# Optimization experiments

Measured on AMD Instinct MI355X. Metric: run time of the kernel, lower is better.

The kernel has to match this reference:

```python
import jax, jax.numpy as jnp
import numpy as np

H = 1024        # hidden_size
NH = 16         # num_heads
HD = H // NH    # head_dim
NS = 3          # num_strata


def setup_inputs() -> dict:
    key = jax.random.key(0)
    ks = jax.random.split(key, 12)
    s = 1.0 / np.sqrt(H)
    inp = {
        "hidden_states": jax.random.normal(ks[0], (2, 2048, H), dtype=jnp.float32),
        "Wq": jax.random.uniform(ks[1], (H, H), minval=-s, maxval=s, dtype=jnp.float32),
        "bq": jax.random.uniform(ks[2], (H,), minval=-s, maxval=s, dtype=jnp.float32),
        "Wk": jax.random.uniform(ks[3], (H, H), minval=-s, maxval=s, dtype=jnp.float32),
        "bk": jax.random.uniform(ks[4], (H,), minval=-s, maxval=s, dtype=jnp.float32),
        "Wv": jax.random.uniform(ks[5], (H, H), minval=-s, maxval=s, dtype=jnp.float32),
        "bv": jax.random.uniform(ks[6], (H,), minval=-s, maxval=s, dtype=jnp.float32),
        "Ws": jax.random.uniform(ks[7], (NS, H, H), minval=-s, maxval=s, dtype=jnp.float32),
        "bs": jax.random.uniform(ks[8], (NS, H), minval=-s, maxval=s, dtype=jnp.float32),
        "Wo": jax.random.uniform(ks[9], (H, H), minval=-s, maxval=s, dtype=jnp.float32),
        "bo": jax.random.uniform(ks[10], (H,), minval=-s, maxval=s, dtype=jnp.float32),
    }
    return inp


def reference(hidden_states, Wq, bq, Wk, bk, Wv, bv, Ws, bs, Wo, bo):
    B, S, _ = hidden_states.shape
    # torch nn.Linear: y = x @ W.T + b
    q = hidden_states @ Wq.T + bq
    k = hidden_states @ Wk.T + bk
    v = hidden_states @ Wv.T + bv
    # [B, NH, S, HD]
    q = q.reshape(B, S, NH, HD).transpose(0, 2, 1, 3)
    k = k.reshape(B, S, NH, HD).transpose(0, 2, 1, 3)
    v = v.reshape(B, S, NH, HD).transpose(0, 2, 1, 3)
    scores = jnp.einsum('bhqd,bhkd->bhqk', q, k) / jnp.sqrt(jnp.float32(HD))
    attn = jax.nn.softmax(scores, axis=-1)
    out = jnp.einsum('bhqk,bhkd->bhqd', attn, v)
    attn_output = out.transpose(0, 2, 1, 3).reshape(B, S, H)
    # stratum projections, averaged: [NS, B, S, H] -> mean over strata
    strata = jnp.einsum('bsh,ngh->nbsg', attn_output, Ws) + bs[:, None, None, :]
    enhanced = strata.mean(axis=0)
    output = enhanced @ Wo.T + bo
    return output
```

## Files before the change

kernel.cpp:

```cpp
#include <hip/hip_runtime.h>
#include <stdint.h>

typedef __attribute__((ext_vector_type(8))) short short8;
typedef __attribute__((ext_vector_type(4))) short short4v;
typedef __attribute__((ext_vector_type(4))) float f32x4;
typedef __attribute__((ext_vector_type(16))) float f32x16;
typedef __attribute__((ext_vector_type(2))) unsigned int u32x2;
typedef __attribute__((ext_vector_type(4))) unsigned int u32x4;
typedef unsigned int u32;
typedef const __attribute__((address_space(1))) u32* gas_ptr;
typedef __attribute__((address_space(3))) u32* las_ptr;

#define QSCALE 0.18033688011112042f

__device__ inline short f2bf(float x) {
    u32 u = __float_as_uint(x);
    u = u + 0x7FFFu + ((u >> 16) & 1u);
    return (short)(u >> 16);
}
__device__ inline void gload16(const void* g, const void* l) {
    __builtin_amdgcn_global_load_lds((gas_ptr)g, (las_ptr)l, 16, 0, 0);
}

__global__ __launch_bounds__(256) void prep(const float* __restrict__ X,
                                            const float* __restrict__ Wq,
                                            const float* __restrict__ Wk,
                                            const float* __restrict__ Wv,
                                            const float* __restrict__ Wo,
                                            const float* __restrict__ Ws,
                                            const float* __restrict__ bs,
                                            const float* __restrict__ bo,
                                            short* __restrict__ Xb,
                                            short* __restrict__ Wcat,
                                            short* __restrict__ Wob,
                                            short* __restrict__ WmT,
                                            float* __restrict__ bc) {
    __shared__ short T[64][65];
    const int tid = threadIdx.x;
    const int bid = blockIdx.x;
    if (bid < 2048) {
#pragma unroll
        for (int c = 0; c < 4; c++) {
            const int chunk = bid * 4 + c;
            const float* src;
            short* dst;
            int rel;
            if (chunk < 4096)      { src = X;  dst = Xb;                rel = chunk; }
            else if (chunk < 5120) { src = Wq; dst = Wcat;              rel = chunk - 4096; }
            else if (chunk < 6144) { src = Wk; dst = Wcat + (1 << 20);  rel = chunk - 5120; }
            else if (chunk < 7168) { src = Wv; dst = Wcat + (2 << 20);  rel = chunk - 6144; }
            else                   { src = Wo; dst = Wob;               rel = chunk - 7168; }
            int i = (rel * 256 + tid) * 4;
            float4 v = *(const float4*)&src[i];
            short4v o;
            o[0] = f2bf(v.x); o[1] = f2bf(v.y); o[2] = f2bf(v.z); o[3] = f2bf(v.w);
            *(short4v*)&dst[i] = o;
        }
    } else if (bid < 2304) {
        const int id = bid - 2048;
        const int gx = (id & 15) * 64, jy = (id >> 4) * 64;
        const int HH = 1 << 20;
        for (int e = tid; e < 4096; e += 256) {
            int j = e >> 6, g = e & 63;
            int idx = (jy + j) * 1024 + gx + g;
            float v = (Ws[idx] + Ws[idx + HH] + Ws[idx + 2 * HH]) * (1.0f / 3.0f);
            T[g][j] = f2bf(v);
        }
        __syncthreads();
        for (int e = tid; e < 4096; e += 256) {
            int g = e >> 6, j = e & 63;
            WmT[(long)(gx + g) * 1024 + jy + j] = T[g][j];
        }
    } else {
        const int lane = tid & 63;
        const int n = (bid - 2304) * 4 + (tid >> 6);
        float acc = 0.0f;
        for (int j0 = 0; j0 < 1024; j0 += 64) {
            int j = j0 + lane;
            float bm = (bs[j] + bs[j + 1024] + bs[j + 2048]) * (1.0f / 3.0f);
            acc += Wo[(long)n * 1024 + j] * bm;
        }
#pragma unroll
        for (int off = 1; off < 64; off <<= 1) acc += __shfl_xor(acc, off, 64);
        if (lane == 0) bc[n] = acc + bo[n];
    }
}

__global__ __launch_bounds__(256) void gemm_qkvwc(const short* __restrict__ Xb,
                                                  const short* __restrict__ Wcat,
                                                  const short* __restrict__ Wob,
                                                  const short* __restrict__ WmT,
                                                  const float* __restrict__ bq,
                                                  const float* __restrict__ bk,
                                                  const float* __restrict__ bv,
                                                  short* __restrict__ Qb,
                                                  short* __restrict__ Kb,
                                                  short* __restrict__ Vt,
                                                  short* __restrict__ Wc) {
    __shared__ short As[64 * 64];
    __shared__ short Bs[128 * 64];
    const int K = 1024;
    const int tid  = threadIdx.x;
    const int lane = tid & 63;
    const int wave = tid >> 6;
    const int quad = lane >> 4;
    const int l16  = lane & 15;
    const int bid = (blockIdx.x & 7) * 208 + (blockIdx.x >> 3);
    const short *A, *W;
    int m0, n0, sel;
    if (bid < 1536) {
        sel = bid >> 9;
        int r = bid & 511;
        m0 = (r >> 3) * 64;
        n0 = (r & 7) * 128;
        A = Xb;
        W = Wcat + (long)sel * (1 << 20);
    } else {
        int w = bid - 1536;
        sel = 3;
        m0 = (w >> 3) * 64;
        n0 = (w & 7) * 128;
        A = Wob;
        W = WmT;
    }
    const int wm = (wave >> 1) * 32;
    const int wn = (wave & 1) * 64;

    f32x4 acc[2][4] = {};
    const int sr = tid >> 3;
    const int scol = (((tid & 7) ^ (sr & 7)) << 3);
    const int fo_a = ((quad ^ (l16 & 7)) << 3);
    const int fo_b = (((4 + quad) ^ (l16 & 7)) << 3);

    for (int k0 = 0; k0 < K; k0 += 64) {
#pragma unroll
        for (int i = 0; i < 2; i++) {
            int r = i * 32 + sr;
            gload16(&A[(long)(m0 + r) * K + k0 + scol], &As[i * 2048 + wave * 512]);
        }
#pragma unroll
        for (int i = 0; i < 4; i++) {
            int r = i * 32 + sr;
            gload16(&W[(long)(n0 + r) * K + k0 + scol], &Bs[i * 2048 + wave * 512]);
        }
        __syncthreads();
        short8 bfr[4][2];
#pragma unroll
        for (int ni = 0; ni < 4; ni++) {
            const int row = wn + ni * 16 + l16;
            bfr[ni][0] = *(short8*)&Bs[row * 64 + fo_a];
            bfr[ni][1] = *(short8*)&Bs[row * 64 + fo_b];
        }
#pragma unroll
        for (int mi = 0; mi < 2; mi++) {
            const int row = wm + mi * 16 + l16;
            short8 af0 = *(short8*)&As[row * 64 + fo_a];
            short8 af1 = *(short8*)&As[row * 64 + fo_b];
#pragma unroll
            for (int ni = 0; ni < 4; ni++) {
                acc[mi][ni] = __builtin_amdgcn_mfma_f32_16x16x32_bf16(af0, bfr[ni][0],
                                                                      acc[mi][ni], 0, 0, 0);
                acc[mi][ni] = __builtin_amdgcn_mfma_f32_16x16x32_bf16(af1, bfr[ni][1],
                                                                      acc[mi][ni], 0, 0, 0);
            }
        }
        __syncthreads();
    }

#pragma unroll
    for (int mi = 0; mi < 2; mi++) {
#pragma unroll
        for (int ni = 0; ni < 4; ni++) {
            const int n = n0 + wn + ni * 16 + l16;
            const int mbase = m0 + wm + mi * 16 + quad * 4;
            float bv2 = 0.0f;
            if (sel == 0) bv2 = bq[n];
            else if (sel == 1) bv2 = bk[n];
            else if (sel == 2) bv2 = bv[n];
            if (sel == 2) {
                short4v pk;
#pragma unroll
                for (int r = 0; r < 4; r++) pk[r] = f2bf(acc[mi][ni][r] + bv2);
                long addr = ((long)(mbase >> 11) << 21) + (long)n * 2048 + (mbase & 2047);
                *(short4v*)&Vt[addr] = pk;
            } else if (sel == 0) {
#pragma unroll
                for (int r = 0; r < 4; r++)
                    Qb[(long)(mbase + r) * 1024 + n] = f2bf((acc[mi][ni][r] + bv2) * QSCALE);
            } else {
                short* C = (sel == 1) ? Kb : Wc;
#pragma unroll
                for (int r = 0; r < 4; r++)
                    C[(long)(mbase + r) * 1024 + n] = f2bf(acc[mi][ni][r] + bv2);
            }
        }
    }
}

__global__ __launch_bounds__(512, 4) void attn_kernel(const short* __restrict__ Q,
                                                      const short* __restrict__ Kb,
                                                      const short* __restrict__ Vt,
                                                      short* __restrict__ O) {
    __shared__ short Ks[2][2][64 * 64];
    __shared__ short Vs[2][64 * 64];
    const int tid   = threadIdx.x;
    const int lane  = tid & 63;
    const int wave  = tid >> 6;
    const int group = wave >> 2;
    const int wv    = wave & 3;
    const int gtid  = tid & 255;
    const int l32   = lane & 31;
    const int hi    = lane >> 5;
    const int sw    = l32 & 7;
    const int q0 = blockIdx.x * 128;
    const int h  = blockIdx.y;
    const int b  = blockIdx.z;

    short8 qB[4];
    {
        const long qbase = (long)(b * 2048 + q0 + wv * 32 + l32) * 1024 + h * 64 + hi * 8;
#pragma unroll
        for (int t = 0; t < 4; t++) qB[t] = *(const short8*)&Q[qbase + t * 16];
    }

    const int sr = gtid >> 3;
    const int scol = (((gtid & 7) ^ (sr & 7)) << 3);
    const short* Kp = Kb + (long)(b * 2048 + group * 1024) * 1024 + h * 64;
    const short* Vp = Vt + ((long)b << 21) + (long)h * 64 * 2048 + group * 1024;

    f32x16 o[2] = {};
    float lsum = 0.0f;

#pragma unroll
    for (int i = 0; i < 2; i++) {
        int r = i * 32 + sr;
        gload16(&Kp[(long)r * 1024 + scol], &Ks[group][0][i * 2048 + wv * 512]);
    }
    __syncthreads();

    for (int kt = 0; kt < 16; kt++) {
        const int cur = kt & 1;
        const int kb = kt * 64;

#pragma unroll
        for (int i = 0; i < 2; i++) {
            int r = i * 32 + sr;
            gload16(&Vp[(long)r * 2048 + kb + scol], &Vs[group][i * 2048 + wv * 512]);
        }

        u32 c0[8], c1[8];
#pragma unroll
        for (int kvt = 0; kvt < 2; kvt++) {
            const int row = kvt * 32 + l32;
            f32x16 st = {};
            __builtin_amdgcn_s_setprio(1);
#pragma unroll
            for (int step = 0; step < 4; step++) {
                short8 ak = *(short8*)&Ks[group][cur][row * 64 + (((step * 2 + hi) ^ sw) << 3)];
                st = __builtin_amdgcn_mfma_f32_32x32x16_bf16(ak, qB[step], st, 0, 0, 0);
            }
            __builtin_amdgcn_s_setprio(0);
#pragma unroll
            for (int g = 0; g < 4; g++) {
                float p0 = __builtin_amdgcn_exp2f(st[g * 4 + 0]);
                float p1 = __builtin_amdgcn_exp2f(st[g * 4 + 1]);
                float p2 = __builtin_amdgcn_exp2f(st[g * 4 + 2]);
                float p3 = __builtin_amdgcn_exp2f(st[g * 4 + 3]);
                lsum += (p0 + p1) + (p2 + p3);
                u32 w0, w1;
                asm("v_cvt_pk_bf16_f32 %0, %1, %2" : "=v"(w0) : "v"(p0), "v"(p1));
                asm("v_cvt_pk_bf16_f32 %0, %1, %2" : "=v"(w1) : "v"(p2), "v"(p3));
                c0[kvt * 4 + g] = w0;
                c1[kvt * 4 + g] = w1;
            }
        }

        __syncthreads();

        if (kt < 15) {
            const int kbn = kb + 64;
#pragma unroll
            for (int i = 0; i < 2; i++) {
                int r = i * 32 + sr;
                gload16(&Kp[(long)(kbn + r) * 1024 + scol],
                        &Ks[group][cur ^ 1][i * 2048 + wv * 512]);
            }
        }

        short8 pB[4];
#pragma unroll
        for (int s = 0; s < 4; s++) {
            u32x2 r0 = __builtin_amdgcn_permlane32_swap(c0[2 * s], c0[2 * s + 1], false, false);
            u32x2 r1 = __builtin_amdgcn_permlane32_swap(c1[2 * s], c1[2 * s + 1], false, false);
            u32x4 bw;
            bw[0] = r0[0]; bw[1] = r1[0]; bw[2] = r0[1]; bw[3] = r1[1];
            pB[s] = __builtin_bit_cast(short8, bw);
        }

        __builtin_amdgcn_s_setprio(1);
#pragma unroll
        for (int dt = 0; dt < 2; dt++) {
            const int row = dt * 32 + l32;
#pragma unroll
            for (int s = 0; s < 4; s++) {
                short8 av = *(short8*)&Vs[group][row * 64 + (((s * 2 + hi) ^ sw) << 3)];
                o[dt] = __builtin_amdgcn_mfma_f32_32x32x16_bf16(av, pB[s], o[dt], 0, 0, 0);
            }
        }
        __builtin_amdgcn_s_setprio(0);

        __syncthreads();
    }

    lsum += __shfl_xor(lsum, 32, 64);
    float* cb = (float*)&Ks[0][0][0];
    float* lb = (float*)&Vs[0][0];
    const int ql = wv * 32 + l32;
    if (group == 1) {
#pragma unroll
        for (int dt = 0; dt < 2; dt++) {
#pragma unroll
            for (int g = 0; g < 4; g++) {
                f32x4 v4;
#pragma unroll
                for (int i = 0; i < 4; i++) v4[i] = o[dt][g * 4 + i];
                *(f32x4*)&cb[ql * 64 + dt * 32 + g * 8 + hi * 4] = v4;
            }
        }
        if (hi == 0) lb[ql] = lsum;
    }
    __syncthreads();
    if (group == 0) {
        const float inv = 1.0f / (lsum + lb[ql]);
        const long rbase = (long)(b * 2048 + q0 + ql) * 1024 + h * 64;
#pragma unroll
        for (int dt = 0; dt < 2; dt++) {
#pragma unroll
            for (int g = 0; g < 4; g++) {
                const f32x4 pv = *(const f32x4*)&cb[ql * 64 + dt * 32 + g * 8 + hi * 4];
                short4v pk;
#pragma unroll
                for (int i = 0; i < 4; i++) pk[i] = f2bf((o[dt][g * 4 + i] + pv[i]) * inv);
                *(short4v*)&O[rbase + dt * 32 + g * 8 + hi * 4] = pk;
            }
        }
    }
}

__global__ __launch_bounds__(256) void gemm_final(const short* __restrict__ A,
                                                  const short* __restrict__ W,
                                                  const float* __restrict__ bias,
                                                  float* __restrict__ C) {
    __shared__ short As[64 * 64];
    __shared__ short Bs[128 * 64];
    const int K = 1024;
    const int tid  = threadIdx.x;
    const int lane = tid & 63;
    const int wave = tid >> 6;
    const int quad = lane >> 4;
    const int l16  = lane & 15;
    const int bid = (blockIdx.x & 7) * 64 + (blockIdx.x >> 3);
    const int m0 = (bid >> 3) * 64;
    const int n0 = (bid & 7) * 128;
    const int wm = (wave >> 1) * 32;
    const int wn = (wave & 1) * 64;

    f32x4 acc[2][4] = {};
    const int sr = tid >> 3;
    const int scol = (((tid & 7) ^ (sr & 7)) << 3);
    const int fo_a = ((quad ^ (l16 & 7)) << 3);
    const int fo_b = (((4 + quad) ^ (l16 & 7)) << 3);

    for (int k0 = 0; k0 < K; k0 += 64) {
#pragma unroll
        for (int i = 0; i < 2; i++) {
            int r = i * 32 + sr;
            gload16(&A[(long)(m0 + r) * K + k0 + scol], &As[i * 2048 + wave * 512]);
        }
#pragma unroll
        for (int i = 0; i < 4; i++) {
            int r = i * 32 + sr;
            gload16(&W[(long)(n0 + r) * K + k0 + scol], &Bs[i * 2048 + wave * 512]);
        }
        __syncthreads();
        short8 bfr[4][2];
#pragma unroll
        for (int ni = 0; ni < 4; ni++) {
            const int row = wn + ni * 16 + l16;
            bfr[ni][0] = *(short8*)&Bs[row * 64 + fo_a];
            bfr[ni][1] = *(short8*)&Bs[row * 64 + fo_b];
        }
#pragma unroll
        for (int mi = 0; mi < 2; mi++) {
            const int row = wm + mi * 16 + l16;
            short8 af0 = *(short8*)&As[row * 64 + fo_a];
            short8 af1 = *(short8*)&As[row * 64 + fo_b];
#pragma unroll
            for (int ni = 0; ni < 4; ni++) {
                acc[mi][ni] = __builtin_amdgcn_mfma_f32_16x16x32_bf16(af0, bfr[ni][0],
                                                                      acc[mi][ni], 0, 0, 0);
                acc[mi][ni] = __builtin_amdgcn_mfma_f32_16x16x32_bf16(af1, bfr[ni][1],
                                                                      acc[mi][ni], 0, 0, 0);
            }
        }
        __syncthreads();
    }

#pragma unroll
    for (int mi = 0; mi < 2; mi++) {
#pragma unroll
        for (int ni = 0; ni < 4; ni++) {
            const int n = n0 + wn + ni * 16 + l16;
            const float bv = bias[n];
            const int mbase = m0 + wm + mi * 16 + quad * 4;
#pragma unroll
            for (int r = 0; r < 4; r++)
                C[(long)(mbase + r) * 1024 + n] = acc[mi][ni][r] + bv;
        }
    }
}

extern "C" void kernel_launch(void* const* d_in, const int* in_sizes, int n_in,
                              void* d_out, int out_size, void* d_ws, size_t ws_size,
                              hipStream_t stream) {
    const float* X  = (const float*)d_in[0];
    const float* Wq = (const float*)d_in[1];
    const float* bq = (const float*)d_in[2];
    const float* Wk = (const float*)d_in[3];
    const float* bk = (const float*)d_in[4];
    const float* Wv = (const float*)d_in[5];
    const float* bv = (const float*)d_in[6];
    const float* Ws = (const float*)d_in[7];
    const float* bs = (const float*)d_in[8];
    const float* Wo = (const float*)d_in[9];
    const float* bo = (const float*)d_in[10];

    char* ws = (char*)d_ws;
    const long MB = 1 << 20;
    short* Xb   = (short*)(ws + 0 * MB);
    short* Wcat = (short*)(ws + 8 * MB);
    short* WmT  = (short*)(ws + 14 * MB);
    short* Wob  = (short*)(ws + 16 * MB);
    short* Wc   = (short*)(ws + 18 * MB);
    float* bc   = (float*)(ws + 20 * MB);
    short* Qb   = (short*)(ws + 21 * MB);
    short* Kbf  = (short*)(ws + 29 * MB);
    short* Vtb  = (short*)(ws + 37 * MB);
    short* AO   = Xb;

    dim3 bb(256);

    prep<<<dim3(2560), bb, 0, stream>>>(X, Wq, Wk, Wv, Wo, Ws, bs, bo,
                                        Xb, Wcat, Wob, WmT, bc);
    gemm_qkvwc<<<dim3(1664), bb, 0, stream>>>(Xb, Wcat, Wob, WmT, bq, bk, bv,
                                              Qb, Kbf, Vtb, Wc);
    attn_kernel<<<dim3(16, 16, 2), dim3(512), 0, stream>>>(Qb, Kbf, Vtb, AO);
    gemm_final<<<dim3(512), bb, 0, stream>>>(AO, Wc, bc, (float*)d_out);
}
```

Measured before the change: 205.3 us.

## Fuse all four stages into one cooperative persistent kernel with grid syncs

Replaces the four separate launches (prep, QKV/Wc GEMM, attention, final GEMM) with a single cooperative kernel of 512 blocks × 512 threads. Stages are separated by grid.sync, and each block runs two 256-thread sub-tiles in the GEMM phases. This removes launch gaps and inter-kernel drain, but the fixed grid lowers per-stage parallelism, which risks underutilisation and stalls at the grid barriers. It falls back to the old path if occupancy or the cooperative launch fails.

New measurement: 205.5 us. Within noise of the previous version (+0.1%).

```diff
diff --git a/kernel.cpp b/kernel.cpp
--- a/kernel.cpp
+++ b/kernel.cpp
@@ -1,5 +1,8 @@
 #include <hip/hip_runtime.h>
+#include <hip/hip_cooperative_groups.h>
 #include <stdint.h>
+
+namespace cg = cooperative_groups;
 
 typedef __attribute__((ext_vector_type(8))) short short8;
 typedef __attribute__((ext_vector_type(4))) short short4v;
@@ -20,6 +23,411 @@
 }
 __device__ inline void gload16(const void* g, const void* l) {
     __builtin_amdgcn_global_load_lds((gas_ptr)g, (las_ptr)l, 16, 0, 0);
+}
+
+__global__ __launch_bounds__(512, 4) void mega(
+    const float* __restrict__ X,  const float* __restrict__ Wq, const float* __restrict__ bq,
+    const float* __restrict__ Wk, const float* __restrict__ bk,
+    const float* __restrict__ Wv, const float* __restrict__ bv,
+    const float* __restrict__ Ws, const float* __restrict__ bs,
+    const float* __restrict__ Wo, const float* __restrict__ bo,
+    short* __restrict__ Xb, short* __restrict__ Wcat, short* __restrict__ Wob,
+    short* __restrict__ WmT, float* __restrict__ bc,
+    short* __restrict__ Qb, short* __restrict__ Kb2, short* __restrict__ Vt,
+    short* __restrict__ Wc, float* __restrict__ out)
+{
+    __shared__ __align__(16) char smem[49152];
+    cg::grid_group grid = cg::this_grid();
+    const int tid  = threadIdx.x;
+    const int blk  = blockIdx.x;
+    const int half = tid >> 8;
+    const int gt   = tid & 255;
+    const int grp  = (blk << 1) | half;
+
+    {
+        for (int u = grp; u < 8192; u += 1024) {
+            const float* src; short* dst; int rel;
+            if (u < 4096)      { src = X;  dst = Xb;               rel = u; }
+            else if (u < 5120) { src = Wq; dst = Wcat;             rel = u - 4096; }
+            else if (u < 6144) { src = Wk; dst = Wcat + (1 << 20); rel = u - 5120; }
+            else if (u < 7168) { src = Wv; dst = Wcat + (2 << 20); rel = u - 6144; }
+            else               { src = Wo; dst = Wob;              rel = u - 7168; }
+            int i = (rel * 256 + gt) * 4;
+            float4 v = *(const float4*)&src[i];
+            short4v o;
+            o[0] = f2bf(v.x); o[1] = f2bf(v.y); o[2] = f2bf(v.z); o[3] = f2bf(v.w);
+            *(short4v*)&dst[i] = o;
+        }
+        {
+            short* T = (short*)(smem + half * 8448);
+            const bool act2 = grp < 256;
+            const int gx = (grp & 15) * 64, jy = ((grp >> 4) & 15) * 64;
+            const int HH = 1 << 20;
+            if (act2) {
+                for (int e = gt; e < 4096; e += 256) {
+                    int j = e >> 6, g = e & 63;
+                    int idx = (jy + j) * 1024 + gx + g;
+                    float v = (Ws[idx] + Ws[idx + HH] + Ws[idx + 2 * HH]) * (1.0f / 3.0f);
+                    T[g * 65 + j] = f2bf(v);
+                }
+            }
+            __syncthreads();
+            if (act2) {
+                for (int e = gt; e < 4096; e += 256) {
+                    int g = e >> 6, j = e & 63;
+                    WmT[(long)(gx + g) * 1024 + jy + j] = T[g * 65 + j];
+                }
+            }
+        }
+        {
+            const int w = blk * 8 + (tid >> 6);
+            if (w < 1024) {
+                const int lane = tid & 63;
+                float acc = 0.0f;
+                for (int j0 = 0; j0 < 1024; j0 += 64) {
+                    int j = j0 + lane;
+                    float bm = (bs[j] + bs[j + 1024] + bs[j + 2048]) * (1.0f / 3.0f);
+                    acc += Wo[(long)w * 1024 + j] * bm;
+                }
+#pragma unroll
+                for (int off = 1; off < 64; off <<= 1) acc += __shfl_xor(acc, off, 64);
+                if (lane == 0) bc[w] = acc + bo[w];
+            }
+        }
+    }
+    __threadfence();
+    grid.sync();
+    __threadfence();
+
+    {
+        short* As = (short*)(smem + half * 24576);
+        short* Bs = As + 4096;
+        const int lane = gt & 63, wave = gt >> 6;
+        const int quad = lane >> 4, l16 = lane & 15;
+        const int wm = (wave >> 1) * 32, wn = (wave & 1) * 64;
+        const int sr = gt >> 3;
+        const int scol = (((gt & 7) ^ (sr & 7)) << 3);
+        const int fo_a = ((quad ^ (l16 & 7)) << 3);
+        const int fo_b = (((4 + quad) ^ (l16 & 7)) << 3);
+        const int xcd = blk & 7;
+        const int lcl = ((blk >> 3) << 1) | half;
+#pragma unroll 1
+        for (int pass = 0; pass < 2; pass++) {
+            const int loc = pass * 128 + lcl;
+            const bool act = loc < 208;
+            const int u = xcd * 208 + loc;
+            const short* A = Xb;
+            const short* W = Wcat;
+            int m0 = 0, n0 = 0, sel = 0;
+            if (act) {
+                if (u < 1536) {
+                    sel = u >> 9;
+                    int r = u & 511;
+                    m0 = (r >> 3) * 64;
+                    n0 = (r & 7) * 128;
+                    A = Xb;
+                    W = Wcat + (long)sel * (1 << 20);
+                } else {
+                    int w2 = u - 1536;
+                    sel = 3;
+                    m0 = (w2 >> 3) * 64;
+                    n0 = (w2 & 7) * 128;
+                    A = Wob;
+                    W = WmT;
+                }
+            }
+            f32x4 acc[2][4] = {};
+            for (int k0 = 0; k0 < 1024; k0 += 64) {
+                if (act) {
+#pragma unroll
+                    for (int i = 0; i < 2; i++)
+                        gload16(&A[(long)(m0 + i * 32 + sr) * 1024 + k0 + scol],
+                                &As[i * 2048 + wave * 512]);
+#pragma unroll
+                    for (int i = 0; i < 4; i++)
+                        gload16(&W[(long)(n0 + i * 32 + sr) * 1024 + k0 + scol],
+                                &Bs[i * 2048 + wave * 512]);
+                }
+                __syncthreads();
+                if (act) {
+                    short8 bfr[4][2];
+#pragma unroll
+                    for (int ni = 0; ni < 4; ni++) {
+                        const int row = wn + ni * 16 + l16;
+                        bfr[ni][0] = *(short8*)&Bs[row * 64 + fo_a];
+                        bfr[ni][1] = *(short8*)&Bs[row * 64 + fo_b];
+                    }
+#pragma unroll
+                    for (int mi = 0; mi < 2; mi++) {
+                        const int row = wm + mi * 16 + l16;
+                        short8 af0 = *(short8*)&As[row * 64 + fo_a];
+                        short8 af1 = *(short8*)&As[row * 64 + fo_b];
+#pragma unroll
+                        for (int ni = 0; ni < 4; ni++) {
+                            acc[mi][ni] = __builtin_amdgcn_mfma_f32_16x16x32_bf16(
+                                af0, bfr[ni][0], acc[mi][ni], 0, 0, 0);
+                            acc[mi][ni] = __builtin_amdgcn_mfma_f32_16x16x32_bf16(
+                                af1, bfr[ni][1], acc[mi][ni], 0, 0, 0);
+                        }
+                    }
+                }
+                __syncthreads();
+            }
+            if (act) {
+#pragma unroll
+                for (int mi = 0; mi < 2; mi++) {
+#pragma unroll
+                    for (int ni = 0; ni < 4; ni++) {
+                        const int n = n0 + wn + ni * 16 + l16;
+                        const int mbase = m0 + wm + mi * 16 + quad * 4;
+                        float bv2 = 0.0f;
+                        if (sel == 0) bv2 = bq[n];
+                        else if (sel == 1) bv2 = bk[n];
+                        else if (sel == 2) bv2 = bv[n];
+                        if (sel == 2) {
+                            short4v pk;
+#pragma unroll
+                            for (int r = 0; r < 4; r++) pk[r] = f2bf(acc[mi][ni][r] + bv2);
+                            long addr = ((long)(mbase >> 11) << 21) + (long)n * 2048 + (mbase & 2047);
+                            *(short4v*)&Vt[addr] = pk;
+                        } else if (sel == 0) {
+#pragma unroll
+                            for (int r = 0; r < 4; r++)
+                                Qb[(long)(mbase + r) * 1024 + n] = f2bf((acc[mi][ni][r] + bv2) * QSCALE);
+                        } else {
+                            short* C = (sel == 1) ? Kb2 : Wc;
+#pragma unroll
+                            for (int r = 0; r < 4; r++)
+                                C[(long)(mbase + r) * 1024 + n] = f2bf(acc[mi][ni][r] + bv2);
+                        }
+                    }
+                }
+            }
+        }
+    }
+    __threadfence();
+    grid.sync();
+    __threadfence();
+
+    {
+        short* KsB = (short*)smem;
+        short* VsB = (short*)(smem + 32768);
+        const int lane  = tid & 63;
+        const int wave  = tid >> 6;
+        const int group = wave >> 2;
+        const int wv    = wave & 3;
+        const int gtid  = tid & 255;
+        const int l32   = lane & 31;
+        const int hi    = lane >> 5;
+        const int sw    = l32 & 7;
+        const int q0 = (blk & 15) * 128;
+        const int h  = (blk >> 4) & 15;
+        const int b  = blk >> 8;
+
+        short8 qB[4];
+        {
+            const long qbase = (long)(b * 2048 + q0 + wv * 32 + l32) * 1024 + h * 64 + hi * 8;
+#pragma unroll
+            for (int t = 0; t < 4; t++) qB[t] = *(const short8*)&Qb[qbase + t * 16];
+        }
+        const int sr = gtid >> 3;
+        const int scol = (((gtid & 7) ^ (sr & 7)) << 3);
+        const short* Kp = Kb2 + (long)(b * 2048 + group * 1024) * 1024 + h * 64;
+        const short* Vp = Vt + ((long)b << 21) + (long)h * 64 * 2048 + group * 1024;
+
+        f32x16 o[2] = {};
+        float lsum = 0.0f;
+
+#pragma unroll
+        for (int i = 0; i < 2; i++) {
+            int r = i * 32 + sr;
+            gload16(&Kp[(long)r * 1024 + scol], &KsB[(group << 1) * 4096 + i * 2048 + wv * 512]);
+        }
+        __syncthreads();
+
+        for (int kt = 0; kt < 16; kt++) {
+            const int cur = kt & 1;
+            const int kb = kt * 64;
+            short* Kcur = &KsB[((group << 1) | cur) * 4096];
+            short* Vg   = &VsB[group * 4096];
+
+#pragma unroll
+            for (int i = 0; i < 2; i++) {
+                int r = i * 32 + sr;
+                gload16(&Vp[(long)r * 2048 + kb + scol], &Vg[i * 2048 + wv * 512]);
+            }
+
+            u32 c0[8], c1[8];
+#pragma unroll
+            for (int kvt = 0; kvt < 2; kvt++) {
+                const int row = kvt * 32 + l32;
+                f32x16 st = {};
+                __builtin_amdgcn_s_setprio(1);
+#pragma unroll
+                for (int step = 0; step < 4; step++) {
+                    short8 ak = *(short8*)&Kcur[row * 64 + (((step * 2 + hi) ^ sw) << 3)];
+                    st = __builtin_amdgcn_mfma_f32_32x32x16_bf16(ak, qB[step], st, 0, 0, 0);
+                }
+                __builtin_amdgcn_s_setprio(0);
+#pragma unroll
+                for (int g = 0; g < 4; g++) {
+                    float p0 = __builtin_amdgcn_exp2f(st[g * 4 + 0]);
+                    float p1 = __builtin_amdgcn_exp2f(st[g * 4 + 1]);
+                    float p2 = __builtin_amdgcn_exp2f(st[g * 4 + 2]);
+                    float p3 = __builtin_amdgcn_exp2f(st[g * 4 + 3]);
+                    lsum += (p0 + p1) + (p2 + p3);
+                    u32 w0, w1;
+                    asm("v_cvt_pk_bf16_f32 %0, %1, %2" : "=v"(w0) : "v"(p0), "v"(p1));
+                    asm("v_cvt_pk_bf16_f32 %0, %1, %2" : "=v"(w1) : "v"(p2), "v"(p3));
+                    c0[kvt * 4 + g] = w0;
+                    c1[kvt * 4 + g] = w1;
+                }
+            }
+
+            __syncthreads();
+
+            if (kt < 15) {
+                const int kbn = kb + 64;
+                short* Knext = &KsB[((group << 1) | (cur ^ 1)) * 4096];
+#pragma unroll
+                for (int i = 0; i < 2; i++) {
+                    int r = i * 32 + sr;
+                    gload16(&Kp[(long)(kbn + r) * 1024 + scol], &Knext[i * 2048 + wv * 512]);
+                }
+            }
+
+            short8 pB[4];
+#pragma unroll
+            for (int s = 0; s < 4; s++) {
+                u32x2 r0 = __builtin_amdgcn_permlane32_swap(c0[2 * s], c0[2 * s + 1], false, false);
+                u32x2 r1 = __builtin_amdgcn_permlane32_swap(c1[2 * s], c1[2 * s + 1], false, false);
+                u32x4 bw;
+                bw[0] = r0[0]; bw[1] = r1[0]; bw[2] = r0[1]; bw[3] = r1[1];
+                pB[s] = __builtin_bit_cast(short8, bw);
+            }
+
+            __builtin_amdgcn_s_setprio(1);
+#pragma unroll
+            for (int dt = 0; dt < 2; dt++) {
+                const int row = dt * 32 + l32;
+#pragma unroll
+                for (int s = 0; s < 4; s++) {
+                    short8 av = *(short8*)&Vg[row * 64 + (((s * 2 + hi) ^ sw) << 3)];
+                    o[dt] = __builtin_amdgcn_mfma_f32_32x32x16_bf16(av, pB[s], o[dt], 0, 0, 0);
+                }
+            }
+            __builtin_amdgcn_s_setprio(0);
+
+            __syncthreads();
+        }
+
+        lsum += __shfl_xor(lsum, 32, 64);
+        float* cb = (float*)smem;
+        float* lb = (float*)(smem + 32768);
+        const int ql = wv * 32 + l32;
+        if (group == 1) {
+#pragma unroll
+            for (int dt = 0; dt < 2; dt++) {
+#pragma unroll
+                for (int g = 0; g < 4; g++) {
+                    f32x4 v4;
+#pragma unroll
+                    for (int i = 0; i < 4; i++) v4[i] = o[dt][g * 4 + i];
+                    *(f32x4*)&cb[ql * 64 + dt * 32 + g * 8 + hi * 4] = v4;
+                }
+            }
+            if (hi == 0) lb[ql] = lsum;
+        }
+        __syncthreads();
+        if (group == 0) {
+            const float inv = 1.0f / (lsum + lb[ql]);
+            const long rbase = (long)(b * 2048 + q0 + ql) * 1024 + h * 64;
+#pragma unroll
+            for (int dt = 0; dt < 2; dt++) {
+#pragma unroll
+                for (int g = 0; g < 4; g++) {
+                    const f32x4 pv = *(const f32x4*)&cb[ql * 64 + dt * 32 + g * 8 + hi * 4];
+                    short4v pk;
+#pragma unroll
+                    for (int i = 0; i < 4; i++) pk[i] = f2bf((o[dt][g * 4 + i] + pv[i]) * inv);
+                    *(short4v*)&Xb[rbase + dt * 32 + g * 8 + hi * 4] = pk;
+                }
+            }
+        }
+    }
+    __threadfence();
+    grid.sync();
+    __threadfence();
+
+    {
+        short* As = (short*)(smem + half * 24576);
+        short* Bs = As + 4096;
+        const int lane = gt & 63, wave = gt >> 6;
+        const int quad = lane >> 4, l16 = lane & 15;
+        const int wm = (wave >> 1) * 32, wn = (wave & 1) * 64;
+        const int sr = gt >> 3;
+        const int scol = (((gt & 7) ^ (sr & 7)) << 3);
+        const int fo_a = ((quad ^ (l16 & 7)) << 3);
+        const int fo_b = (((4 + quad) ^ (l16 & 7)) << 3);
+        const int xcd = blk & 7;
+        const int lcl = ((blk >> 3) << 1) | half;
+        const bool act = lcl < 64;
+        const int u = xcd * 64 + lcl;
+        const int m0 = (u >> 3) * 64;
+        const int n0 = (u & 7) * 128;
+
+        f32x4 acc[2][4] = {};
+        for (int k0 = 0; k0 < 1024; k0 += 64) {
+            if (act) {
+#pragma unroll
+                for (int i = 0; i < 2; i++)
+                    gload16(&Xb[(long)(m0 + i * 32 + sr) * 1024 + k0 + scol],
+                            &As[i * 2048 + wave * 512]);
+#pragma unroll
+                for (int i = 0; i < 4; i++)
+                    gload16(&Wc[(long)(n0 + i * 32 + sr) * 1024 + k0 + scol],
+                            &Bs[i * 2048 + wave * 512]);
+            }
+            __syncthreads();
+            if (act) {
+                short8 bfr[4][2];
+#pragma unroll
+                for (int ni = 0; ni < 4; ni++) {
+                    const int row = wn + ni * 16 + l16;
+                    bfr[ni][0] = *(short8*)&Bs[row * 64 + fo_a];
+                    bfr[ni][1] = *(short8*)&Bs[row * 64 + fo_b];
+                }
+#pragma unroll
+                for (int mi = 0; mi < 2; mi++) {
+                    const int row = wm + mi * 16 + l16;
+                    short8 af0 = *(short8*)&As[row * 64 + fo_a];
+                    short8 af1 = *(short8*)&As[row * 64 + fo_b];
+#pragma unroll
+                    for (int ni = 0; ni < 4; ni++) {
+                        acc[mi][ni] = __builtin_amdgcn_mfma_f32_16x16x32_bf16(
+                            af0, bfr[ni][0], acc[mi][ni], 0, 0, 0);
+                        acc[mi][ni] = __builtin_amdgcn_mfma_f32_16x16x32_bf16(
+                            af1, bfr[ni][1], acc[mi][ni], 0, 0, 0);
+                    }
+                }
+            }
+            __syncthreads();
+        }
+        if (act) {
+#pragma unroll
+            for (int mi = 0; mi < 2; mi++) {
+#pragma unroll
+                for (int ni = 0; ni < 4; ni++) {
+                    const int n = n0 + wn + ni * 16 + l16;
+                    const float bv2 = bc[n];
+                    const int mbase = m0 + wm + mi * 16 + quad * 4;
+#pragma unroll
+                    for (int r = 0; r < 4; r++)
+                        out[(long)(mbase + r) * 1024 + n] = acc[mi][ni][r] + bv2;
+                }
+            }
+        }
+    }
 }
 
 __global__ __launch_bounds__(256) void prep(const float* __restrict__ X,
@@ -446,14 +854,41 @@
     short* Qb   = (short*)(ws + 21 * MB);
     short* Kbf  = (short*)(ws + 29 * MB);
     short* Vtb  = (short*)(ws + 37 * MB);
-    short* AO   = Xb;
-
-    dim3 bb(256);
-
-    prep<<<dim3(2560), bb, 0, stream>>>(X, Wq, Wk, Wv, Wo, Ws, bs, bo,
-                                        Xb, Wcat, Wob, WmT, bc);
-    gemm_qkvwc<<<dim3(1664), bb, 0, stream>>>(Xb, Wcat, Wob, WmT, bq, bk, bv,
-                                              Qb, Kbf, Vtb, Wc);
-    attn_kernel<<<dim3(16, 16, 2), dim3(512), 0, stream>>>(Qb, Kbf, Vtb, AO);
-    gemm_final<<<dim3(512), bb, 0, stream>>>(AO, Wc, bc, (float*)d_out);
+    float* outp = (float*)d_out;
+
+    static int coop_ok = -1;
+    if (coop_ok < 0) {
+        int maxb = 0;
+        hipError_t qe = hipOccupancyMaxActiveBlocksPerMultiprocessor(
+            &maxb, (const void*)mega, 512, 0);
+        coop_ok = (qe == hipSuccess && maxb >= 2) ? 1 : 0;
+    }
+
+    bool launched = false;
+    if (coop_ok == 1) {
+        void* args[] = {
+            (void*)&X,  (void*)&Wq, (void*)&bq, (void*)&Wk, (void*)&bk,
+            (void*)&Wv, (void*)&bv, (void*)&Ws, (void*)&bs, (void*)&Wo, (void*)&bo,
+            (void*)&Xb, (void*)&Wcat, (void*)&Wob, (void*)&WmT, (void*)&bc,
+            (void*)&Qb, (void*)&Kbf, (void*)&Vtb, (void*)&Wc, (void*)&outp
+        };
+        hipError_t le = hipLaunchCooperativeKernel((const void*)mega, dim3(512), dim3(512),
+                                                   args, 0, stream);
+        if (le == hipSuccess) {
+            launched = true;
+        } else {
+            (void)hipGetLastError();
+            coop_ok = 0;
+        }
+    }
+
+    if (!launched) {
+        dim3 bb(256);
+        prep<<<dim3(2560), bb, 0, stream>>>(X, Wq, Wk, Wv, Wo, Ws, bs, bo,
+                                            Xb, Wcat, Wob, WmT, bc);
+        gemm_qkvwc<<<dim3(1664), bb, 0, stream>>>(Xb, Wcat, Wob, WmT, bq, bk, bv,
+                                                  Qb, Kbf, Vtb, Wc);
+        attn_kernel<<<dim3(16, 16, 2), dim3(512), 0, stream>>>(Qb, Kbf, Vtb, Xb);
+        gemm_final<<<dim3(512), bb, 0, stream>>>(Xb, Wc, bc, outp);
+    }
 }
```
